# Optimization experiments

Hardware: AMD Instinct MI355X
Metric: run time of the kernel (lower is better)

## Reference

```python
import jax, jax.numpy as jnp
import numpy as np

BN_EPS = 1e-5

def tanhshrink(x):
    return x - jnp.tanh(x)

def setup_inputs() -> dict:
    key = jax.random.key(0)
    ks = jax.random.split(key, 10)
    B, C, H, W = 32, 128, 32, 32
    RIN, RH, OC = 256, 512, 128
    s = lambda k, shape, fan: jax.random.normal(k, shape, dtype=jnp.float32) * (1.0 / np.sqrt(fan))
    return {
        "x": jax.random.normal(ks[0], (B, C, H, W), dtype=jnp.float32),
        "gamma": jnp.ones((C,), jnp.float32),
        "beta": jnp.zeros((C,), jnp.float32),
        "w_in": s(ks[1], (RIN, C), C),
        "b_in": jnp.zeros((RIN,), jnp.float32),
        "w_ih": s(ks[2], (RH, RIN), RIN),
        "b_ih": jnp.zeros((RH,), jnp.float32),
        "w_hh": s(ks[3], (RH, RH), RH),
        "b_hh": jnp.zeros((RH,), jnp.float32),
        "w_out": s(ks[4], (OC, RH), RH),
        "b_out": jnp.zeros((OC,), jnp.float32),
    }

def reference(x, gamma, beta, w_in, b_in, w_ih, b_ih, w_hh, b_hh, w_out, b_out):
    B, C, H, W = x.shape
    RH = w_hh.shape[0]
    # BatchNorm2d (training mode: batch statistics, biased variance)
    mean = jnp.mean(x, axis=(0, 2, 3), keepdims=True)
    var = jnp.var(x, axis=(0, 2, 3), keepdims=True)
    xn = (x - mean) * jax.lax.rsqrt(var + BN_EPS)
    xn = xn * gamma[None, :, None, None] + beta[None, :, None, None]
    # (B, L, C) sequence of flattened spatial locations
    seq = jnp.transpose(xn, (0, 2, 3, 1)).reshape(B, H * W, C)
    # Per-timestep Linear + Tanhshrink: has no recurrence, batch it over L
    inp = tanhshrink(jnp.einsum('blc,ic->bli', seq, w_in) + b_in)  # (B, L, RIN)
    # Precompute input contribution to RNNCell for all steps
    xgate = jnp.einsum('bli,hi->blh', inp, w_ih) + b_ih + b_hh  # (B, L, RH)
    xgate_t = jnp.transpose(xgate, (1, 0, 2))  # (L, B, RH)

    def step(h, xg):
        h_new = jnp.tanh(xg + h @ w_hh.T)
        return h_new, h_new

    h0 = jnp.zeros((B, RH), x.dtype)
    _, hs = jax.lax.scan(step, h0, xgate_t)  # (L, B, RH)
    outputs = jnp.transpose(hs, (1, 0, 2))  # (B, L, RH)
    out_seq = jnp.einsum('blh,oh->blo', outputs, w_out) + b_out  # (B, L, OC)
    out = jnp.transpose(out_seq.reshape(B, H, W, -1), (0, 3, 1, 2))
    return out
```

## Files before the change

kernel.cpp:

```cpp
#include <hip/hip_runtime.h>
#include <hip/hip_fp16.h>

typedef _Float16 f16;
typedef _Float16 f16x2 __attribute__((ext_vector_type(2)));
typedef _Float16 f16x8 __attribute__((ext_vector_type(8)));
typedef float    f32x4 __attribute__((ext_vector_type(4)));
typedef unsigned int u32;
typedef unsigned long long u64;

#define BN_EPS 1e-5f

static constexpr int BB  = 32;
static constexpr int CC  = 128;
static constexpr int HWN = 1024;
static constexpr int RIN = 256;
static constexpr int RH  = 512;
static constexpr int OCN = 128;

__global__ void bn_stats_kernel(const float* __restrict__ x,
                                const float* __restrict__ gamma,
                                const float* __restrict__ beta,
                                float* __restrict__ scale,
                                float* __restrict__ shift) {
    int c = blockIdx.x;
    int tid = threadIdx.x;
    float s = 0.f, s2 = 0.f;
    const float* xc = x + (size_t)c * HWN;
    for (int idx = tid; idx < BB * HWN; idx += 256) {
        int b = idx >> 10, hw = idx & 1023;
        float v = xc[(size_t)b * (CC * HWN) + hw];
        s += v; s2 += v * v;
    }
    for (int off = 32; off > 0; off >>= 1) {
        s  += __shfl_down(s, off, 64);
        s2 += __shfl_down(s2, off, 64);
    }
    __shared__ float ls[4], ls2[4];
    int wv = tid >> 6, ln = tid & 63;
    if (ln == 0) { ls[wv] = s; ls2[wv] = s2; }
    __syncthreads();
    if (tid == 0) {
        float ts  = ls[0] + ls[1] + ls[2] + ls[3];
        float ts2 = ls2[0] + ls2[1] + ls2[2] + ls2[3];
        const float inv_n = 1.0f / (BB * HWN);
        float mean = ts * inv_n;
        float var  = ts2 * inv_n - mean * mean;
        float rstd = rsqrtf(var + BN_EPS);
        float sc = gamma[c] * rstd;
        scale[c] = sc;
        shift[c] = beta[c] - mean * sc;
    }
}

__global__ void prep_x_kernel(const float* __restrict__ x,
                              const float* __restrict__ scale,
                              const float* __restrict__ shift,
                              f16* __restrict__ A1) {
    __shared__ float tile[32][33];
    int tx = threadIdx.x, ty = threadIdx.y;
    int hb = blockIdx.x, cb = blockIdx.y, b = blockIdx.z;
    #pragma unroll
    for (int k = 0; k < 4; k++) {
        int c  = cb * 32 + ty + 8 * k;
        int hw = hb * 32 + tx;
        tile[ty + 8 * k][tx] = x[(size_t)b * (CC * HWN) + (size_t)c * HWN + hw];
    }
    __syncthreads();
    #pragma unroll
    for (int k = 0; k < 4; k++) {
        int hw = hb * 32 + ty + 8 * k;
        int c  = cb * 32 + tx;
        float v = tile[tx][ty + 8 * k];
        A1[(size_t)(b * HWN + hw) * CC + c] = (f16)(v * scale[c] + shift[c]);
    }
}

__global__ void prep_w_kernel(const float* __restrict__ w_in,
                              const float* __restrict__ w_ih,
                              const float* __restrict__ w_out,
                              const float* __restrict__ w_hh,
                              const float* __restrict__ b_ih,
                              const float* __restrict__ b_hh,
                              f16* __restrict__ w_in_h,
                              f16* __restrict__ w_ih_h,
                              f16* __restrict__ w_out_h,
                              u32* __restrict__ wr,
                              float* __restrict__ bihh,
                              u32* __restrict__ comm) {
    int idx = blockIdx.x * 256 + threadIdx.x;
    if (idx < 32768) { w_in_h[idx] = (f16)w_in[idx]; return; }
    idx -= 32768;
    if (idx < 131072) { w_ih_h[idx] = (f16)w_ih[idx]; return; }
    idx -= 131072;
    if (idx < 65536) { w_out_h[idx] = (f16)w_out[idx]; return; }
    idx -= 65536;
    if (idx < 131072) {
        int s = idx >> 14, rem = idx & 16383;
        int t = rem >> 5, w = rem & 31;
        int r = t >> 3, c = t & 7;
        int i = w >> 2, k = w & 3;
        int i2 = c * 32 + 4 * (i ^ c) + k;
        int j  = s * 64 + r;
        f16 lo = (f16)w_hh[(size_t)j * 512 + 2 * i2];
        f16 hi = (f16)w_hh[(size_t)j * 512 + 2 * i2 + 1];
        wr[idx] = (u32)__builtin_bit_cast(unsigned short, lo) |
                  ((u32)__builtin_bit_cast(unsigned short, hi) << 16);
        return;
    }
    idx -= 131072;
    if (idx < 512) { bihh[idx] = b_ih[idx] + b_hh[idx]; return; }
    idx -= 512;
    if (idx < 32768) comm[idx] = 0u;
}

template <int MODE>
__global__ void gemm_kernel(const f16* __restrict__ A,
                            const f16* __restrict__ W,
                            const float* __restrict__ bias,
                            void* __restrict__ outp,
                            int N, int K) {
    int wave = threadIdx.x >> 6;
    int lane = threadIdx.x & 63;
    int q = lane >> 4, r = lane & 15;
    int bm = blockIdx.x * 256 + wave * 64;
    int bn = blockIdx.y * 64;

    f32x4 acc[4][4];
    #pragma unroll
    for (int i = 0; i < 4; i++)
        #pragma unroll
        for (int j = 0; j < 4; j++)
            acc[i][j] = (f32x4){0.f, 0.f, 0.f, 0.f};

    const f16* Ap = A + (size_t)(bm + r) * K + 8 * q;
    const f16* Wp = W + (size_t)(bn + r) * K + 8 * q;

    for (int k = 0; k < K; k += 32) {
        f16x8 av[4], bv[4];
        #pragma unroll
        for (int i = 0; i < 4; i++)
            av[i] = *(const f16x8*)(Ap + (size_t)(16 * i) * K + k);
        #pragma unroll
        for (int i = 0; i < 4; i++)
            bv[i] = *(const f16x8*)(Wp + (size_t)(16 * i) * K + k);
        #pragma unroll
        for (int mi = 0; mi < 4; mi++)
            #pragma unroll
            for (int ni = 0; ni < 4; ni++)
                acc[mi][ni] = __builtin_amdgcn_mfma_f32_16x16x32_f16(
                    av[mi], bv[ni], acc[mi][ni], 0, 0, 0);
    }

    #pragma unroll
    for (int mi = 0; mi < 4; mi++) {
        #pragma unroll
        for (int ni = 0; ni < 4; ni++) {
            int col = bn + 16 * ni + r;
            float bval = bias[col];
            #pragma unroll
            for (int i = 0; i < 4; i++) {
                int row = bm + 16 * mi + 4 * q + i;
                float val = acc[mi][ni][i] + bval;
                if (MODE == 0) {
                    val = val - tanhf(val);
                    ((f16*)outp)[(size_t)row * N + col] = (f16)val;
                } else if (MODE == 1) {
                    ((f16*)outp)[(size_t)row * N + col] = (f16)val;
                } else {
                    int b = row >> 10, hw = row & 1023;
                    ((float*)outp)[(size_t)b * (OCN * HWN) + (size_t)col * HWN + hw] = val;
                }
            }
        }
    }
}

__device__ __forceinline__ float dot2acc(u32 w, f16x2 h, float c) {
#if __has_builtin(__builtin_amdgcn_fdot2)
    return __builtin_amdgcn_fdot2(__builtin_bit_cast(f16x2, w), h, c, false);
#else
    f16x2 a = __builtin_bit_cast(f16x2, w);
    return c + (float)a[0] * (float)h[0] + (float)a[1] * (float)h[1];
#endif
}

__device__ __forceinline__ f16x2 u2h(u32 w) { return __builtin_bit_cast(f16x2, w); }

__global__ void __launch_bounds__(512)
__attribute__((amdgpu_waves_per_eu(2, 2)))
rnn_kernel(const u32* WR, f16* __restrict__ xh, u32* comm) {
    const int wg = blockIdx.x;
    const int b  = wg & 31;
    const int s  = wg >> 5;
    const int t  = threadIdx.x;
    const int r  = t >> 3;
    const int c  = t & 7;
    const bool leader = (c == 0);

    __shared__ __align__(16) f16 hbuf[2][512];

    const uint4* wp = (const uint4*)(WR + ((size_t)(s * 512 + t) << 5));
    uint4 q0_ = wp[0], q1_ = wp[1], q2_ = wp[2], q3_ = wp[3];
    uint4 q4_ = wp[4], q5_ = wp[5], q6_ = wp[6], q7_ = wp[7];
    u32 W00 = q0_.x, W01 = q0_.y, W02 = q0_.z, W03 = q0_.w;
    u32 W04 = q1_.x, W05 = q1_.y, W06 = q1_.z, W07 = q1_.w;
    u32 W08 = q2_.x, W09 = q2_.y, W10 = q2_.z, W11 = q2_.w;
    u32 W12 = q3_.x, W13 = q3_.y, W14 = q3_.z, W15 = q3_.w;
    u32 W16 = q4_.x, W17 = q4_.y, W18 = q4_.z, W19 = q4_.w;
    u32 W20 = q5_.x, W21 = q5_.y, W22 = q5_.z, W23 = q5_.w;
    u32 W24 = q6_.x, W25 = q6_.y, W26 = q6_.z, W27 = q6_.w;
    u32 W28 = q7_.x, W29 = q7_.y, W30 = q7_.z, W31 = q7_.w;
    asm volatile("" : "+v"(W00), "+v"(W01), "+v"(W02), "+v"(W03),
                      "+v"(W04), "+v"(W05), "+v"(W06), "+v"(W07),
                      "+v"(W08), "+v"(W09), "+v"(W10), "+v"(W11),
                      "+v"(W12), "+v"(W13), "+v"(W14), "+v"(W15));
    asm volatile("" : "+v"(W16), "+v"(W17), "+v"(W18), "+v"(W19),
                      "+v"(W20), "+v"(W21), "+v"(W22), "+v"(W23),
                      "+v"(W24), "+v"(W25), "+v"(W26), "+v"(W27),
                      "+v"(W28), "+v"(W29), "+v"(W30), "+v"(W31));

    ((u32*)hbuf)[t] = 0u;
    __syncthreads();

    f16* xg = xh + (size_t)b * (HWN * RH) + s * 64 + r;
    float xnext = leader ? (float)xg[0] : 0.f;

    const bool isPoller = (t >= 64);
    const int pi = (t - 64) >> 6;
    const int pp = pi + (pi >= s ? 1 : 0);
    const int pj = t & 63;

    const char* hb0 = (const char*)&hbuf[0][0];
    const int cbyte = c << 7;

    for (int step = 0; step < HWN; step++) {
        const u32 tag  = (u32)(step + 1);
        const int nxt  = (int)(tag & 1);
        const char* hb = hb0 + ((step & 1) << 10);

        u32* paddr = comm + ((size_t)(tag & 1) << 14) + ((size_t)b << 9)
                          + (pp << 6) + pj;
        u32 vpre = 0;
        if (isPoller)
            vpre = __hip_atomic_load(paddr, __ATOMIC_RELAXED, __HIP_MEMORY_SCOPE_AGENT);

        float xcur = xnext;
        if (leader && step + 1 < HWN)
            xnext = (float)xg[(size_t)(step + 1) * RH];

        float aA = 0.f, aB = 0.f, aC = 0.f, aD = 0.f;
        #define GRP(i, ACC, Wa, Wb, Wc, Wd)                                   \
        {   uint4 q = *(const uint4*)(hb + (cbyte | (((i) ^ c) << 4)));       \
            ACC = dot2acc(Wa, u2h(q.x), ACC);                                 \
            ACC = dot2acc(Wb, u2h(q.y), ACC);                                 \
            ACC = dot2acc(Wc, u2h(q.z), ACC);                                 \
            ACC = dot2acc(Wd, u2h(q.w), ACC); }
        GRP(0, aA, W00, W01, W02, W03)
        GRP(1, aB, W04, W05, W06, W07)
        GRP(2, aC, W08, W09, W10, W11)
        GRP(3, aD, W12, W13, W14, W15)
        GRP(4, aA, W16, W17, W18, W19)
        GRP(5, aB, W20, W21, W22, W23)
        GRP(6, aC, W24, W25, W26, W27)
        GRP(7, aD, W28, W29, W30, W31)
        #undef GRP
        float acc = (aA + aB) + (aC + aD);
        acc += __shfl_xor(acc, 1, 64);
        acc += __shfl_xor(acc, 2, 64);
        acc += __shfl_xor(acc, 4, 64);

        if (leader) {
            float h = tanhf(xcur + acc);
            f16 hf = (f16)h;
            u32 word = (tag << 16) | (u32)__builtin_bit_cast(unsigned short, hf);
            __hip_atomic_store(comm + ((size_t)(tag & 1) << 14) + ((size_t)b << 9)
                                    + (s << 6) + r,
                               word, __ATOMIC_RELAXED, __HIP_MEMORY_SCOPE_AGENT);
            hbuf[nxt][(s << 6) + r] = hf;
            xg[(size_t)step * RH] = hf;
        }
        if (isPoller) {
            u32 v = vpre;
            if ((v >> 16) != tag) {
                u32 v2 = __hip_atomic_load(paddr, __ATOMIC_RELAXED, __HIP_MEMORY_SCOPE_AGENT);
                int guard = 0;
                while ((v >> 16) != tag && ++guard < (1 << 17)) {
                    v = v2;
                    v2 = __hip_atomic_load(paddr, __ATOMIC_RELAXED, __HIP_MEMORY_SCOPE_AGENT);
                }
            }
            hbuf[nxt][(pp << 6) + pj] =
                __builtin_bit_cast(f16, (unsigned short)(v & 0xFFFFu));
        }
        __syncthreads();
    }
}

extern "C" void kernel_launch(void* const* d_in, const int* in_sizes, int n_in,
                              void* d_out, int out_size, void* d_ws, size_t ws_size,
                              hipStream_t stream) {
    const float* x     = (const float*)d_in[0];
    const float* gamma = (const float*)d_in[1];
    const float* beta  = (const float*)d_in[2];
    const float* w_in  = (const float*)d_in[3];
    const float* b_in  = (const float*)d_in[4];
    const float* w_ih  = (const float*)d_in[5];
    const float* b_ih  = (const float*)d_in[6];
    const float* w_hh  = (const float*)d_in[7];
    const float* b_hh  = (const float*)d_in[8];
    const float* w_out = (const float*)d_in[9];
    const float* b_out = (const float*)d_in[10];

    char* ws = (char*)d_ws;
    float* scale   = (float*)(ws + 0);
    float* shift   = (float*)(ws + 512);
    float* bihh    = (float*)(ws + 1024);
    f16*   w_in_h  = (f16*)(ws + 4096);
    f16*   w_ih_h  = (f16*)(ws + 69632);
    f16*   w_out_h = (f16*)(ws + 331776);
    u32*   wr      = (u32*)(ws + 462848);
    u32*   comm    = (u32*)(ws + 987136);
    f16*   xh      = (f16*)(ws + 1179648);
    f16*   A1      = (f16*)(ws + 34734080);
    f16*   inp     = (f16*)(ws + 43122688);

    bn_stats_kernel<<<128, 256, 0, stream>>>(x, gamma, beta, scale, shift);
    prep_w_kernel<<<1538, 256, 0, stream>>>(w_in, w_ih, w_out, w_hh, b_ih, b_hh,
                                            w_in_h, w_ih_h, w_out_h, wr, bihh, comm);
    prep_x_kernel<<<dim3(32, 4, 32), dim3(32, 8), 0, stream>>>(x, scale, shift, A1);
    gemm_kernel<0><<<dim3(128, 4), 256, 0, stream>>>(A1, w_in_h, b_in, (void*)inp, RIN, CC);
    gemm_kernel<1><<<dim3(128, 8), 256, 0, stream>>>(inp, w_ih_h, bihh, (void*)xh, RH, RIN);
    rnn_kernel<<<256, 512, 0, stream>>>(wr, xh, comm);
    gemm_kernel<2><<<dim3(128, 2), 256, 0, stream>>>(xh, w_out_h, b_out, d_out, OCN, RH);
}
```

Baseline: 1.653 ms.

## Run each batch's RNN recurrence in a single workgroup, dropping cross-block polling

The recurrence was split across 8 workgroups per batch element that exchanged hidden-state slices through global atomic flags and spin-polling. It now runs one 512-thread workgroup per batch element, where each thread owns one hidden unit. Half of the W_hh rows are held in registers and the other half are streamed from global/L2 every step, with a transpose-style shuffle reduction across 8 lanes. This removes the inter-block synchronization latency, but the grid shrinks to 32 workgroups and each step reloads 256KB of weights per block.

```diff
diff --git a/kernel.cpp b/kernel.cpp
--- a/kernel.cpp
+++ b/kernel.cpp
@@ -85,8 +85,7 @@
                               f16* __restrict__ w_ih_h,
                               f16* __restrict__ w_out_h,
                               u32* __restrict__ wr,
-                              float* __restrict__ bihh,
-                              u32* __restrict__ comm) {
+                              float* __restrict__ bihh) {
     int idx = blockIdx.x * 256 + threadIdx.x;
     if (idx < 32768) { w_in_h[idx] = (f16)w_in[idx]; return; }
     idx -= 32768;
@@ -95,22 +94,20 @@
     if (idx < 65536) { w_out_h[idx] = (f16)w_out[idx]; return; }
     idx -= 65536;
     if (idx < 131072) {
-        int s = idx >> 14, rem = idx & 16383;
-        int t = rem >> 5, w = rem & 31;
-        int r = t >> 3, c = t & 7;
-        int i = w >> 2, k = w & 3;
-        int i2 = c * 32 + 4 * (i ^ c) + k;
-        int j  = s * 64 + r;
-        f16 lo = (f16)w_hh[(size_t)j * 512 + 2 * i2];
-        f16 hi = (f16)w_hh[(size_t)j * 512 + 2 * i2 + 1];
+        int e = idx & 3, q = idx >> 2;
+        int t = q & 511, slot = q >> 9;
+        int i = slot & 7, j = slot >> 3;
+        int c = t & 7, g = t >> 3;
+        int row = (g << 3) + j;
+        int p = (c << 5) + ((i ^ c) << 2) + e;
+        f16 lo = (f16)w_hh[(size_t)row * 512 + 2 * p];
+        f16 hi = (f16)w_hh[(size_t)row * 512 + 2 * p + 1];
         wr[idx] = (u32)__builtin_bit_cast(unsigned short, lo) |
                   ((u32)__builtin_bit_cast(unsigned short, hi) << 16);
         return;
     }
     idx -= 131072;
     if (idx < 512) { bihh[idx] = b_ih[idx] + b_hh[idx]; return; }
-    idx -= 512;
-    if (idx < 32768) comm[idx] = 0u;
 }
 
 template <int MODE>
@@ -186,112 +183,125 @@
 
 __device__ __forceinline__ f16x2 u2h(u32 w) { return __builtin_bit_cast(f16x2, w); }
 
+#define RQ(n)  uint4 Q##n = wr4[((size_t)(n) << 9) + t];
+#define UP(n)  u32 W##n##x = Q##n.x, W##n##y = Q##n.y, W##n##z = Q##n.z, W##n##w = Q##n.w;
+#define PIN(n) asm volatile("" : "+v"(W##n##x), "+v"(W##n##y), "+v"(W##n##z), "+v"(W##n##w));
+
+#define D4(ACC, Wn, Qh)                                           \
+    ACC = dot2acc(Wn##x, u2h(Qh.x), ACC);                         \
+    ACC = dot2acc(Wn##y, u2h(Qh.y), ACC);                         \
+    ACC = dot2acc(Wn##z, u2h(Qh.z), ACC);                         \
+    ACC = dot2acc(Wn##w, u2h(Qh.w), ACC);
+#define DROW_R(ACC, n0,n1,n2,n3,n4,n5,n6,n7)                      \
+    D4(ACC, W##n0, q0) D4(ACC, W##n1, q1) D4(ACC, W##n2, q2)      \
+    D4(ACC, W##n3, q3) D4(ACC, W##n4, q4) D4(ACC, W##n5, q5)      \
+    D4(ACC, W##n6, q6) D4(ACC, W##n7, q7)
+
+#define DS4(ACC, S, Qh)                                           \
+    ACC = dot2acc(S.x, u2h(Qh.x), ACC);                           \
+    ACC = dot2acc(S.y, u2h(Qh.y), ACC);                           \
+    ACC = dot2acc(S.z, u2h(Qh.z), ACC);                           \
+    ACC = dot2acc(S.w, u2h(Qh.w), ACC);
+#define SLD(v, base)                                              \
+    uint4 v##0 = *(const uint4*)(base + o0);                      \
+    uint4 v##1 = *(const uint4*)(base + o1);                      \
+    uint4 v##2 = *(const uint4*)(base + o2);                      \
+    uint4 v##3 = *(const uint4*)(base + o3);                      \
+    uint4 v##4 = *(const uint4*)(base + o4);                      \
+    uint4 v##5 = *(const uint4*)(base + o5);                      \
+    uint4 v##6 = *(const uint4*)(base + o6);                      \
+    uint4 v##7 = *(const uint4*)(base + o7);
+#define DROW_S(ACC, v)                                            \
+    DS4(ACC, v##0, q0) DS4(ACC, v##1, q1) DS4(ACC, v##2, q2)      \
+    DS4(ACC, v##3, q3) DS4(ACC, v##4, q4) DS4(ACC, v##5, q5)      \
+    DS4(ACC, v##6, q6) DS4(ACC, v##7, q7)
+
 __global__ void __launch_bounds__(512)
 __attribute__((amdgpu_waves_per_eu(2, 2)))
-rnn_kernel(const u32* WR, f16* __restrict__ xh, u32* comm) {
-    const int wg = blockIdx.x;
-    const int b  = wg & 31;
-    const int s  = wg >> 5;
-    const int t  = threadIdx.x;
-    const int r  = t >> 3;
-    const int c  = t & 7;
-    const bool leader = (c == 0);
+rnn_kernel(const u32* WR, f16* __restrict__ xh) {
+    const int b = blockIdx.x;
+    const int t = threadIdx.x;
+    const int c = t & 7;
 
     __shared__ __align__(16) f16 hbuf[2][512];
 
-    const uint4* wp = (const uint4*)(WR + ((size_t)(s * 512 + t) << 5));
-    uint4 q0_ = wp[0], q1_ = wp[1], q2_ = wp[2], q3_ = wp[3];
-    uint4 q4_ = wp[4], q5_ = wp[5], q6_ = wp[6], q7_ = wp[7];
-    u32 W00 = q0_.x, W01 = q0_.y, W02 = q0_.z, W03 = q0_.w;
-    u32 W04 = q1_.x, W05 = q1_.y, W06 = q1_.z, W07 = q1_.w;
-    u32 W08 = q2_.x, W09 = q2_.y, W10 = q2_.z, W11 = q2_.w;
-    u32 W12 = q3_.x, W13 = q3_.y, W14 = q3_.z, W15 = q3_.w;
-    u32 W16 = q4_.x, W17 = q4_.y, W18 = q4_.z, W19 = q4_.w;
-    u32 W20 = q5_.x, W21 = q5_.y, W22 = q5_.z, W23 = q5_.w;
-    u32 W24 = q6_.x, W25 = q6_.y, W26 = q6_.z, W27 = q6_.w;
-    u32 W28 = q7_.x, W29 = q7_.y, W30 = q7_.z, W31 = q7_.w;
-    asm volatile("" : "+v"(W00), "+v"(W01), "+v"(W02), "+v"(W03),
-                      "+v"(W04), "+v"(W05), "+v"(W06), "+v"(W07),
-                      "+v"(W08), "+v"(W09), "+v"(W10), "+v"(W11),
-                      "+v"(W12), "+v"(W13), "+v"(W14), "+v"(W15));
-    asm volatile("" : "+v"(W16), "+v"(W17), "+v"(W18), "+v"(W19),
-                      "+v"(W20), "+v"(W21), "+v"(W22), "+v"(W23),
-                      "+v"(W24), "+v"(W25), "+v"(W26), "+v"(W27),
-                      "+v"(W28), "+v"(W29), "+v"(W30), "+v"(W31));
+    const uint4* wr4 = (const uint4*)WR;
+    RQ(0)  RQ(1)  RQ(2)  RQ(3)  RQ(4)  RQ(5)  RQ(6)  RQ(7)
+    RQ(8)  RQ(9)  RQ(10) RQ(11) RQ(12) RQ(13) RQ(14) RQ(15)
+    RQ(16) RQ(17) RQ(18) RQ(19) RQ(20) RQ(21) RQ(22) RQ(23)
+    RQ(24) RQ(25) RQ(26) RQ(27) RQ(28) RQ(29) RQ(30) RQ(31)
+    UP(0)  UP(1)  UP(2)  UP(3)  UP(4)  UP(5)  UP(6)  UP(7)
+    UP(8)  UP(9)  UP(10) UP(11) UP(12) UP(13) UP(14) UP(15)
+    UP(16) UP(17) UP(18) UP(19) UP(20) UP(21) UP(22) UP(23)
+    UP(24) UP(25) UP(26) UP(27) UP(28) UP(29) UP(30) UP(31)
+    PIN(0)  PIN(1)  PIN(2)  PIN(3)  PIN(4)  PIN(5)  PIN(6)  PIN(7)
+    PIN(8)  PIN(9)  PIN(10) PIN(11) PIN(12) PIN(13) PIN(14) PIN(15)
+    PIN(16) PIN(17) PIN(18) PIN(19) PIN(20) PIN(21) PIN(22) PIN(23)
+    PIN(24) PIN(25) PIN(26) PIN(27) PIN(28) PIN(29) PIN(30) PIN(31)
 
     ((u32*)hbuf)[t] = 0u;
     __syncthreads();
 
-    f16* xg = xh + (size_t)b * (HWN * RH) + s * 64 + r;
-    float xnext = leader ? (float)xg[0] : 0.f;
-
-    const bool isPoller = (t >= 64);
-    const int pi = (t - 64) >> 6;
-    const int pp = pi + (pi >= s ? 1 : 0);
-    const int pj = t & 63;
+    f16* xg = xh + (size_t)b * (HWN * RH);
+
+    const char* sb4 = (const char*)WR + 262144;
+    const char* sb5 = sb4 + 65536;
+    const char* sb6 = sb4 + 131072;
+    const char* sb7 = sb4 + 196608;
+    u32 o0 = (u32)(t << 4);
+    u32 o1 = o0 + 8192,  o2 = o0 + 16384, o3 = o0 + 24576,
+        o4 = o0 + 32768, o5 = o0 + 40960, o6 = o0 + 49152, o7 = o0 + 57344;
 
     const char* hb0 = (const char*)&hbuf[0][0];
-    const int cbyte = c << 7;
+    const int cb = c << 7;
+    const bool s0 = (c & 1) != 0, s1 = (c & 2) != 0, s2 = (c & 4) != 0;
 
     for (int step = 0; step < HWN; step++) {
-        const u32 tag  = (u32)(step + 1);
-        const int nxt  = (int)(tag & 1);
+        asm volatile("" : "+v"(o0), "+v"(o1), "+v"(o2), "+v"(o3),
+                          "+v"(o4), "+v"(o5), "+v"(o6), "+v"(o7));
+        SLD(v4, sb4) SLD(v5, sb5) SLD(v6, sb6) SLD(v7, sb7)
+
+        float xcur = (float)xg[(size_t)step * RH + t];
+
         const char* hb = hb0 + ((step & 1) << 10);
-
-        u32* paddr = comm + ((size_t)(tag & 1) << 14) + ((size_t)b << 9)
-                          + (pp << 6) + pj;
-        u32 vpre = 0;
-        if (isPoller)
-            vpre = __hip_atomic_load(paddr, __ATOMIC_RELAXED, __HIP_MEMORY_SCOPE_AGENT);
-
-        float xcur = xnext;
-        if (leader && step + 1 < HWN)
-            xnext = (float)xg[(size_t)(step + 1) * RH];
-
-        float aA = 0.f, aB = 0.f, aC = 0.f, aD = 0.f;
-        #define GRP(i, ACC, Wa, Wb, Wc, Wd)                                   \
-        {   uint4 q = *(const uint4*)(hb + (cbyte | (((i) ^ c) << 4)));       \
-            ACC = dot2acc(Wa, u2h(q.x), ACC);                                 \
-            ACC = dot2acc(Wb, u2h(q.y), ACC);                                 \
-            ACC = dot2acc(Wc, u2h(q.z), ACC);                                 \
-            ACC = dot2acc(Wd, u2h(q.w), ACC); }
-        GRP(0, aA, W00, W01, W02, W03)
-        GRP(1, aB, W04, W05, W06, W07)
-        GRP(2, aC, W08, W09, W10, W11)
-        GRP(3, aD, W12, W13, W14, W15)
-        GRP(4, aA, W16, W17, W18, W19)
-        GRP(5, aB, W20, W21, W22, W23)
-        GRP(6, aC, W24, W25, W26, W27)
-        GRP(7, aD, W28, W29, W30, W31)
-        #undef GRP
-        float acc = (aA + aB) + (aC + aD);
-        acc += __shfl_xor(acc, 1, 64);
-        acc += __shfl_xor(acc, 2, 64);
-        acc += __shfl_xor(acc, 4, 64);
-
-        if (leader) {
-            float h = tanhf(xcur + acc);
-            f16 hf = (f16)h;
-            u32 word = (tag << 16) | (u32)__builtin_bit_cast(unsigned short, hf);
-            __hip_atomic_store(comm + ((size_t)(tag & 1) << 14) + ((size_t)b << 9)
-                                    + (s << 6) + r,
-                               word, __ATOMIC_RELAXED, __HIP_MEMORY_SCOPE_AGENT);
-            hbuf[nxt][(s << 6) + r] = hf;
-            xg[(size_t)step * RH] = hf;
-        }
-        if (isPoller) {
-            u32 v = vpre;
-            if ((v >> 16) != tag) {
-                u32 v2 = __hip_atomic_load(paddr, __ATOMIC_RELAXED, __HIP_MEMORY_SCOPE_AGENT);
-                int guard = 0;
-                while ((v >> 16) != tag && ++guard < (1 << 17)) {
-                    v = v2;
-                    v2 = __hip_atomic_load(paddr, __ATOMIC_RELAXED, __HIP_MEMORY_SCOPE_AGENT);
-                }
-            }
-            hbuf[nxt][(pp << 6) + pj] =
-                __builtin_bit_cast(f16, (unsigned short)(v & 0xFFFFu));
-        }
+        uint4 q0 = *(const uint4*)(hb + (cb | (((0) ^ c) << 4)));
+        uint4 q1 = *(const uint4*)(hb + (cb | (((1) ^ c) << 4)));
+        uint4 q2 = *(const uint4*)(hb + (cb | (((2) ^ c) << 4)));
+        uint4 q3 = *(const uint4*)(hb + (cb | (((3) ^ c) << 4)));
+        uint4 q4 = *(const uint4*)(hb + (cb | (((4) ^ c) << 4)));
+        uint4 q5 = *(const uint4*)(hb + (cb | (((5) ^ c) << 4)));
+        uint4 q6 = *(const uint4*)(hb + (cb | (((6) ^ c) << 4)));
+        uint4 q7 = *(const uint4*)(hb + (cb | (((7) ^ c) << 4)));
+
+        float a0 = 0.f, a1 = 0.f, a2 = 0.f, a3 = 0.f;
+        DROW_R(a0, 0,1,2,3,4,5,6,7)
+        DROW_R(a1, 8,9,10,11,12,13,14,15)
+        DROW_R(a2, 16,17,18,19,20,21,22,23)
+        DROW_R(a3, 24,25,26,27,28,29,30,31)
+        float a4 = 0.f, a5 = 0.f, a6 = 0.f, a7 = 0.f;
+        DROW_S(a4, v4) DROW_S(a5, v5) DROW_S(a6, v6) DROW_S(a7, v7)
+
+        float x01 = __shfl_xor(s0 ? a0 : a1, 1, 64);
+        float n01 = (s0 ? a1 : a0) + x01;
+        float x23 = __shfl_xor(s0 ? a2 : a3, 1, 64);
+        float n23 = (s0 ? a3 : a2) + x23;
+        float x45 = __shfl_xor(s0 ? a4 : a5, 1, 64);
+        float n45 = (s0 ? a5 : a4) + x45;
+        float x67 = __shfl_xor(s0 ? a6 : a7, 1, 64);
+        float n67 = (s0 ? a7 : a6) + x67;
+
+        float xA = __shfl_xor(s1 ? n01 : n23, 2, 64);
+        float mA = (s1 ? n23 : n01) + xA;
+        float xB = __shfl_xor(s1 ? n45 : n67, 2, 64);
+        float mB = (s1 ? n67 : n45) + xB;
+
+        float xC = __shfl_xor(s2 ? mA : mB, 4, 64);
+        float my = (s2 ? mB : mA) + xC;
+
+        float h = tanhf(xcur + my);
+        f16 hf = (f16)h;
+        hbuf[(step & 1) ^ 1][t] = hf;
+        xg[(size_t)step * RH + t] = hf;
         __syncthreads();
     }
 }
@@ -319,17 +329,16 @@
     f16*   w_ih_h  = (f16*)(ws + 69632);
     f16*   w_out_h = (f16*)(ws + 331776);
     u32*   wr      = (u32*)(ws + 462848);
-    u32*   comm    = (u32*)(ws + 987136);
     f16*   xh      = (f16*)(ws + 1179648);
     f16*   A1      = (f16*)(ws + 34734080);
     f16*   inp     = (f16*)(ws + 43122688);
 
     bn_stats_kernel<<<128, 256, 0, stream>>>(x, gamma, beta, scale, shift);
-    prep_w_kernel<<<1538, 256, 0, stream>>>(w_in, w_ih, w_out, w_hh, b_ih, b_hh,
-                                            w_in_h, w_ih_h, w_out_h, wr, bihh, comm);
+    prep_w_kernel<<<1410, 256, 0, stream>>>(w_in, w_ih, w_out, w_hh, b_ih, b_hh,
+                                            w_in_h, w_ih_h, w_out_h, wr, bihh);
     prep_x_kernel<<<dim3(32, 4, 32), dim3(32, 8), 0, stream>>>(x, scale, shift, A1);
     gemm_kernel<0><<<dim3(128, 4), 256, 0, stream>>>(A1, w_in_h, b_in, (void*)inp, RIN, CC);
     gemm_kernel<1><<<dim3(128, 8), 256, 0, stream>>>(inp, w_ih_h, bihh, (void*)xh, RH, RIN);
-    rnn_kernel<<<256, 512, 0, stream>>>(wr, xh, comm);
+    rnn_kernel<<<32, 512, 0, stream>>>(wr, xh);
     gemm_kernel<2><<<dim3(128, 2), 256, 0, stream>>>(xh, w_out_h, b_out, d_out, OCN, RH);
 }
```

New measurement: 2.943 ms. 1.78x slower.
